# Optimization experiments

Hardware: AMD Instinct MI355X
Metric: run time of the kernel (lower is better)

## Reference

```python
import sys
import jax, jax.numpy as jnp
import numpy as np

sys.setrecursionlimit(100000)

MARGIN = 200.0
SAME_MARGIN = 0.0
REL_MARGIN = MARGIN - SAME_MARGIN  # margin - same_margin


def km_algorithm(mp):
    """Faithful numpy port of the repo's recursive Kuhn-Munkres (host-side,
    exactly mirroring the original CPU round-trip). mp: (n, n) float64.
    Returns transport plan T with T[link[y], y] = 1/n for matched pairs."""
    n = mp.shape[0]
    link = np.full(n, -1, dtype=np.int64)
    lx = mp.max(axis=1).astype(np.float64).copy()
    ly = np.zeros(n, dtype=np.float64)
    st = {}

    def dfs(x):
        st['visx'][x] = True
        for y in range(n):
            if st['visy'][y]:
                continue
            tmp = lx[x] + ly[y] - mp[x, y]
            if abs(tmp) < 1e-5:
                st['visy'][y] = True
                if link[y] == -1 or dfs(link[y]):
                    link[y] = x
                    return True
            elif st['sla'][y] + 1e-5 > tmp:
                st['sla'][y] = tmp
        return False

    for x in range(n):
        st['sla'] = np.full(n, 1e10, dtype=np.float64)
        while True:
            st['visx'] = np.zeros(n, dtype=bool)
            st['visy'] = np.zeros(n, dtype=bool)
            if dfs(x):
                break
            d = st['sla'][~st['visy']].min()
            lx[st['visx']] -= d
            ly[st['visy']] += d
            st['sla'][~st['visy']] -= d
    T = np.zeros((n, n), dtype=np.float64)
    for i in range(n):
        if link[i] != -1:
            T[link[i], i] = 1.0 / n
    return T


def sim_label(l1, l2):
    # (n, n) float: 1 where labels equal
    return (l1[:, None] == l2[None, :]).astype(jnp.float32)


def ground_metric(f1, f2, sim):
    # pairwise squared euclidean distances: ||a||^2 - 2 a.b + ||b||^2
    sq1 = jnp.sum(f1 * f1, axis=1)[:, None]
    sq2 = jnp.sum(f2 * f2, axis=1)[None, :]
    d2 = sq1 - 2.0 * (f1 @ f2.T) + sq2
    hinge_gm = jnp.maximum(0.0, SAME_MARGIN + REL_MARGIN - d2)   # negative pairs
    same_gm = jnp.maximum(0.0, d2 - SAME_MARGIN)                 # positive pairs
    return sim * same_gm + (1.0 - sim) * hinge_gm                # mode='both'


def setup_inputs() -> dict:
    key = jax.random.key(0)
    k1, k2, k3, k4 = jax.random.split(key, 4)
    n, d = 128, 8192
    return {
        "inputs_batch1": jax.random.normal(k1, (n, d), dtype=jnp.float32),
        "inputs_batch2": jax.random.normal(k2, (n, d), dtype=jnp.float32),
        "targets_batch1": jax.random.randint(k3, (n,), 0, 16, dtype=jnp.int64) if jax.config.jax_enable_x64 else jax.random.randint(k3, (n,), 0, 16).astype(jnp.int32),
        "targets_batch2": jax.random.randint(k4, (n,), 0, 16, dtype=jnp.int64) if jax.config.jax_enable_x64 else jax.random.randint(k4, (n,), 0, 16).astype(jnp.int32),
    }


def reference(inputs_batch1, inputs_batch2, targets_batch1, targets_batch2):
    sim = sim_label(targets_batch1, targets_batch2)
    GM = ground_metric(inputs_batch1, inputs_batch2, sim)
    # host round-trip for KM assignment, as in the original module
    T = km_algorithm(np.asarray(jax.device_get(GM), dtype=np.float64))
    T = jnp.asarray(T, dtype=jnp.float32)
    loss = jnp.sum(GM * T)
    return loss
```

## Files before the change

### kernel.cpp

```cpp
#include <hip/hip_runtime.h>

#define N 128
#define DIM 8192
#define NN (N * N)
#define ZSPLIT 64
#define NW 16
#define GSTRIDE 130

__device__ __forceinline__ void wave_fence() {
    __threadfence_block();
    __builtin_amdgcn_wave_barrier();
}
__device__ __forceinline__ double embed_key(double v, int j) {
    long long b = __double_as_longlong(v);
    return __longlong_as_double((b & ~127LL) | (long long)j);
}

__global__ __launch_bounds__(256) void d2_partial(const float* __restrict__ A,
                                                  const float* __restrict__ B,
                                                  float* __restrict__ d2p) {
    __shared__ float As[32][68];
    __shared__ float Bk[64][36];
    const int tid = threadIdx.x;
    const int bi = blockIdx.x, bj = blockIdx.y, bz = blockIdx.z;
    const int tx = tid & 15, ty = tid >> 4;
    const int row0 = bi * 32, col0 = bj * 32;
    const int kbase = bz * 128;
    float a00 = 0.f, a01 = 0.f, a10 = 0.f, a11 = 0.f;

    for (int it = 0; it < 2; ++it) {
        const int k0 = kbase + it * 64;
        __syncthreads();
        #pragma unroll
        for (int s = 0; s < 2; ++s) {
            int e = tid + s * 256;
            int r = e >> 4, q = e & 15;
            *(float4*)&As[r][q * 4] = *(const float4*)&A[(row0 + r) * DIM + k0 + q * 4];
        }
        #pragma unroll
        for (int s = 0; s < 2; ++s) {
            int r = tid & 31;
            int kq = (tid >> 5) + s * 8;
            float4 b4 = *(const float4*)&B[(col0 + r) * DIM + k0 + kq * 4];
            Bk[kq * 4 + 0][r] = b4.x;
            Bk[kq * 4 + 1][r] = b4.y;
            Bk[kq * 4 + 2][r] = b4.z;
            Bk[kq * 4 + 3][r] = b4.w;
        }
        __syncthreads();
        #pragma unroll
        for (int kk = 0; kk < 64; kk += 4) {
            float x0[4], x1[4];
            *(float4*)x0 = *(const float4*)&As[2 * ty][kk];
            *(float4*)x1 = *(const float4*)&As[2 * ty + 1][kk];
            float y[4][2];
            #pragma unroll
            for (int q = 0; q < 4; ++q)
                *(float2*)y[q] = *(const float2*)&Bk[kk + q][2 * tx];
            #pragma unroll
            for (int q = 0; q < 4; ++q) {
                float d;
                d = x0[q] - y[q][0]; a00 = fmaf(d, d, a00);
                d = x0[q] - y[q][1]; a01 = fmaf(d, d, a01);
                d = x1[q] - y[q][0]; a10 = fmaf(d, d, a10);
                d = x1[q] - y[q][1]; a11 = fmaf(d, d, a11);
            }
        }
    }
    const int o0 = (row0 + 2 * ty) * N + col0 + 2 * tx;
    float* dst = d2p + bz * NN;
    *(float2*)&dst[o0]     = make_float2(a00, a01);
    *(float2*)&dst[o0 + N] = make_float2(a10, a11);
}

__global__ __launch_bounds__(256) void reduce_gm(const float* __restrict__ d2p,
                                                 const int* __restrict__ t1,
                                                 const int* __restrict__ t2,
                                                 float* __restrict__ gm,
                                                 int* __restrict__ flagarr) {
    __shared__ int bf;
    if (threadIdx.x == 0) bf = 0;
    __syncthreads();
    const int o = blockIdx.x * 256 + threadIdx.x;
    float s0 = 0.f, s1 = 0.f, s2 = 0.f, s3 = 0.f, s4 = 0.f, s5 = 0.f, s6 = 0.f, s7 = 0.f;
    const float* p = d2p + o;
    #pragma unroll
    for (int z = 0; z < ZSPLIT; z += 8) {
        s0 += p[(z + 0) * NN]; s1 += p[(z + 1) * NN];
        s2 += p[(z + 2) * NN]; s3 += p[(z + 3) * NN];
        s4 += p[(z + 4) * NN]; s5 += p[(z + 5) * NN];
        s6 += p[(z + 6) * NN]; s7 += p[(z + 7) * NN];
    }
    float s = ((s0 + s1) + (s2 + s3)) + ((s4 + s5) + (s6 + s7));
    const int i = o >> 7, j = o & 127;
    const int l1 = t1[i], l2 = t2[j];
    const bool same = (l1 == l2);
    float g = same ? fmaxf(s, 0.f) : fmaxf(200.f - s, 0.f);
    gm[o] = g;
    bool bad = (!same && g > 0.f) || l1 < 0 || l1 > 63 || l2 < 0 || l2 > 63;
    unsigned long long m = __ballot(bad);
    if ((threadIdx.x & 63) == 0 && m) atomicOr(&bf, 1);
    __syncthreads();
    if (threadIdx.x == 0) flagarr[blockIdx.x] = bf;
}

__global__ __launch_bounds__(1024) void solve_kernel(const float* __restrict__ gm,
                                                     const int* __restrict__ flagarr,
                                                     const int* __restrict__ t1,
                                                     const int* __restrict__ t2,
                                                     float* __restrict__ out) {
    __shared__ float gml[N * GSTRIDE];
    __shared__ int lbl1[N], lbl2[N];
    __shared__ int rowlist[N], collist[N];
    __shared__ int rcnt[64], ccnt[64], rstart[65], cstart[65], rcur[64], ccur[64];
    __shared__ int tasks[65], bigtasks[65];
    __shared__ int ntasks_s, nbig_s, flag_s;
    __shared__ double totals[NW];
    __shared__ int claimw[NW][64];
    __shared__ double ub[N + 1], vbp[N + 1], minvb[N + 1];
    __shared__ int pb[N + 1], wayb[N + 1], usedb[N + 1];
    __shared__ double redv[NW];
    __shared__ int redi[NW];
    __shared__ double big_total;
    __shared__ int jfin_s;

    const int tid = threadIdx.x;
    if (tid < 64) { rcnt[tid] = 0; ccnt[tid] = 0; rcur[tid] = 0; ccur[tid] = 0; }
    if (tid == 0) { ntasks_s = 0; nbig_s = 0; flag_s = 0; big_total = 0.0; }
    if (tid < N)  { lbl1[tid] = t1[tid]; lbl2[tid] = t2[tid]; }
    __syncthreads();
    if (tid < 64 && flagarr[tid]) atomicOr(&flag_s, 1);
    if (tid < N) {
        atomicAdd(&rcnt[lbl1[tid] & 63], 1);
        atomicAdd(&ccnt[lbl2[tid] & 63], 1);
    }
    __syncthreads();
    if (tid < 64) {
        int rs_ = rcnt[tid], cs_ = ccnt[tid];
        #pragma unroll
        for (int o = 1; o < 64; o <<= 1) {
            int tr = __shfl_up(rs_, o, 64);
            int tc = __shfl_up(cs_, o, 64);
            if (tid >= o) { rs_ += tr; cs_ += tc; }
        }
        rstart[tid + 1] = rs_;
        cstart[tid + 1] = cs_;
        if (tid == 0) { rstart[0] = 0; cstart[0] = 0; }
        if (!flag_s) {
            int R = rcnt[tid], C = ccnt[tid];
            bool valid = (R > 0) && (C > 0);
            bool small = valid && (R <= 64) && (C <= 64);
            bool big   = valid && !small;
            unsigned long long ms = __ballot(small);
            unsigned long long mb = __ballot(big);
            if (small) tasks[__popcll(ms & ((1ull << tid) - 1))] = tid;
            if (big)   bigtasks[__popcll(mb & ((1ull << tid) - 1))] = tid;
            if (tid == 0) { ntasks_s = __popcll(ms); nbig_s = __popcll(mb); }
        } else if (tid == 0) { ntasks_s = 0; nbig_s = 1; bigtasks[0] = -1; }
    }
    __syncthreads();
    if (tid < N) {
        int l1 = lbl1[tid] & 63;
        int p = atomicAdd(&rcur[l1], 1);
        rowlist[rstart[l1] + p] = tid;
        int l2 = lbl2[tid] & 63;
        int q = atomicAdd(&ccur[l2], 1);
        collist[cstart[l2] + q] = tid;
    }
    __syncthreads();
    #pragma unroll
    for (int pch = 0; pch < 16; ++pch) {
        int e = tid + pch * 1024;
        int i = e >> 7, j = e & 127;
        gml[i * GSTRIDE + j] = gm[rowlist[i] * N + collist[j]];
    }
    __syncthreads();

    const int w = tid >> 6, lane = tid & 63;
    const int ntasks = ntasks_s;
    double acc = 0.0;

    for (int tk = w; tk < ntasks; tk += NW) {
        const int c = tasks[tk];
        const int Rn = rcnt[c], Cn = ccnt[c], rs = rstart[c], cs = cstart[c];
        const bool T  = (Rn > Cn);
        const int n_  = T ? Cn : Rn;
        const int m_  = T ? Rn : Cn;
        const int rstep = T ? 1 : GSTRIDE;
        const int cstep = T ? GSTRIDE : 1;
        const int rb00 = T ? cs : rs * GSTRIDE;
        const int ob00 = T ? rs * GSTRIDE : cs;
        int* clm = claimw[w];

        const bool cA = (lane < m_), rA = (lane < n_);
        const int myoff = ob00 + lane * cstep;
        const int myrb  = rb00 + lane * rstep;

        double u = 0.0;
        if (rA) {
            float mx = 0.f;
            int a = myrb + ob00;
            for (int j = 0; j < m_; ++j) { mx = fmaxf(mx, gml[a]); a += cstep; }
            u = -(double)mx;
        }
        double v = 1e30;
        {
            int a = rb00 + myoff;
            for (int i = 0; i < n_; ++i) {
                double ui = __shfl(u, i, 64);
                if (cA) v = fmin(v, -(double)gml[a] - ui);
                a += rstep;
            }
        }
        if (cA) clm[lane] = 0x7fffffff;
        wave_fence();
        int jc = -1;
        {
            int a = myrb + ob00;
            for (int j = 0; j < m_; ++j) {
                double vj = __shfl(v, j, 64);
                if (rA && jc < 0) {
                    double s = -(double)gml[a] - u - vj;
                    if (s < 1e-7) jc = j;
                }
                a += cstep;
            }
        }
        if (rA && jc >= 0) atomicMin(&clm[jc], lane);
        wave_fence();
        int p = -1;
        if (cA && clm[lane] != 0x7fffffff) p = clm[lane];
        bool rowm = (rA && jc >= 0 && clm[jc] == lane);

        for (int ir = 0; ir < n_; ++ir) {
            if (__shfl(rowm ? 1 : 0, ir, 64)) continue;
            double minv = 1e30, markD = -1.0, ent = -1.0;
            bool used = false; int way = -2;
            if (rA && lane == ir) ent = 0.0;
            double D = 0.0;
            int i0 = ir, jprev = -1;
            int guard = 2 * m_ + 8;
            while (guard-- > 0) {
                double ui = __shfl(u, i0, 64);
                int rb = rb00 + i0 * rstep;
                if (cA && !used) {
                    double cand = D - ui - (double)gml[rb + myoff] - v;
                    if (cand < minv) { minv = cand; way = jprev; }
                }
                double kd = (cA && !used) ? embed_key(minv, lane) : 1e30;
                #pragma unroll
                for (int o = 1; o < 64; o <<= 1) kd = fmin(kd, __shfl_xor(kd, o, 64));
                long long kb = __double_as_longlong(kd);
                int j1 = (int)(kb & 127);
                double Dn = __longlong_as_double(kb & ~127LL);
                if (Dn > 1e29) break;
                D = Dn;
                int i1 = __shfl(p, j1, 64);
                if (i1 < 0) {
                    int jj = j1;
                    while (true) {
                        int wp = __shfl(way, jj, 64);
                        int pn = (wp < 0) ? ir : __shfl(p, wp, 64);
                        if (cA && lane == jj) p = pn;
                        if (wp < 0) break;
                        jj = wp;
                    }
                    if (rA && lane == ir) rowm = true;
                    break;
                }
                if (cA && lane == j1) { used = true; markD = D; }
                if (rA && lane == i1) ent = D;
                jprev = j1; i0 = i1;
            }
            if (rA && ent   >= 0.0) u += D - ent;
            if (cA && markD >= 0.0) v -= D - markD;
        }

        double val = 0.0;
        if (cA && p >= 0) val = (double)gml[rb00 + p * rstep + myoff];
        #pragma unroll
        for (int o = 1; o < 64; o <<= 1) val += __shfl_xor(val, o, 64);
        acc += val;
    }
    if (lane == 0) totals[w] = acc;
    __syncthreads();

    const int nbig = nbig_s;
    for (int bt = 0; bt < nbig; ++bt) {
        const int c = bigtasks[bt];
        int Rn, Cn, rs, cs;
        if (c < 0) { Rn = N; Cn = N; rs = 0; cs = 0; }
        else { Rn = rcnt[c]; Cn = ccnt[c]; rs = rstart[c]; cs = cstart[c]; }
        const bool T = (Rn > Cn);
        const int n_ = T ? Cn : Rn, m_ = T ? Rn : Cn;
        const int rstep = T ? 1 : GSTRIDE;
        const int cstep = T ? GSTRIDE : 1;
        const int rb00 = T ? cs : rs * GSTRIDE;
        const int ob00 = T ? rs * GSTRIDE : cs;
        auto cost = [&](int i, int j) -> double {
            return -(double)gml[rb00 + i * rstep + ob00 + j * cstep];
        };
        for (int x = tid; x <= m_; x += 1024) { vbp[x] = 0.0; pb[x] = 0; }
        for (int x = tid; x <= n_; x += 1024) { ub[x] = 0.0; }
        __syncthreads();
        for (int i = 1; i <= n_; ++i) {
            if (tid == 0) pb[0] = i;
            for (int x = tid; x <= m_; x += 1024) { minvb[x] = 1e300; usedb[x] = 0; }
            __syncthreads();
            int j0 = 0;
            int guard = 2 * m_ + 8;
            while (guard-- > 0) {
                if (tid == 0) usedb[j0] = 1;
                __syncthreads();
                const int i0 = pb[j0];
                double dl = 1e300; int jl = 0;
                if (tid < m_) {
                    int j = tid + 1;
                    if (!usedb[j]) {
                        double cur = cost(i0 - 1, j - 1) - ub[i0] - vbp[j];
                        if (cur < minvb[j]) { minvb[j] = cur; wayb[j] = j0; }
                        dl = minvb[j]; jl = j;
                    }
                }
                double rv = dl; int ri = jl;
                #pragma unroll
                for (int o = 32; o > 0; o >>= 1) {
                    double ov = __shfl_down(rv, o, 64);
                    int oi2 = __shfl_down(ri, o, 64);
                    if (ov < rv) { rv = ov; ri = oi2; }
                }
                if ((tid & 63) == 0) { redv[tid >> 6] = rv; redi[tid >> 6] = ri; }
                __syncthreads();
                if (tid == 0) {
                    double bd = 1e300; int bj = 0;
                    for (int q = 0; q < NW; ++q) if (redv[q] < bd) { bd = redv[q]; bj = redi[q]; }
                    redv[0] = bd; redi[0] = bj;
                }
                __syncthreads();
                const double delta = redv[0];
                const int j1 = redi[0];
                if (tid < m_) {
                    int j = tid + 1;
                    if (usedb[j]) { ub[pb[j]] += delta; vbp[j] -= delta; }
                    else          { minvb[j] -= delta; }
                }
                if (tid == 0) ub[pb[0]] += delta;
                __syncthreads();
                j0 = j1;
                if (pb[j0] == 0) break;
            }
            if (tid == 0) jfin_s = j0;
            __syncthreads();
            if (tid == 0) {
                int jj = jfin_s;
                while (jj) { int jp = wayb[jj]; pb[jj] = pb[jp]; jj = jp; }
            }
            __syncthreads();
        }
        double bl = 0.0;
        if (tid < m_) { int j = tid + 1; if (pb[j] != 0) bl = -cost(pb[j] - 1, j - 1); }
        #pragma unroll
        for (int o = 32; o > 0; o >>= 1) bl += __shfl_down(bl, o, 64);
        if ((tid & 63) == 0) redv[tid >> 6] = bl;
        __syncthreads();
        if (tid == 0) { double s = 0; for (int q = 0; q < NW; ++q) s += redv[q]; big_total += s; }
        __syncthreads();
    }

    if (tid == 0) {
        double s = big_total;
        for (int i = 0; i < NW; ++i) s += totals[i];
        out[0] = (float)(s / (double)N);
    }
}

extern "C" void kernel_launch(void* const* d_in, const int* in_sizes, int n_in,
                              void* d_out, int out_size, void* d_ws, size_t ws_size,
                              hipStream_t stream) {
    const float* A  = (const float*)d_in[0];
    const float* B  = (const float*)d_in[1];
    const int*   t1 = (const int*)d_in[2];
    const int*   t2 = (const int*)d_in[3];
    float* out = (float*)d_out;
    float* d2p = (float*)d_ws;
    float* gm  = (float*)d_ws + ZSPLIT * NN;
    int*   flagarr = (int*)(gm + NN);

    d2_partial<<<dim3(4, 4, ZSPLIT), 256, 0, stream>>>(A, B, d2p);
    reduce_gm<<<64, 256, 0, stream>>>(d2p, t1, t2, gm, flagarr);
    solve_kernel<<<1, 1024, 0, stream>>>(gm, flagarr, t1, t2, out);
}
```

Measured before the change: 90.61 us.

## Use 64x64 tiles with 4x4 register microtiles and finer K split

The squared-distance partial kernel now gives each block a 64x64 output tile over a 64-wide K slice. It loads that slice once and accumulates a 4x4 register microtile per thread, instead of 32x32 tiles with 2x2 microtiles over two 64-wide K steps. The K split grows from 64 to 128 slices and the grid becomes a flat 512 blocks. This halves global reads of A and B and raises arithmetic intensity per shared-memory load. In exchange, the partial-sum buffer doubles, so the reduction kernel reads twice as many partials through new tile-aware indexing.

```diff
diff --git a/kernel.cpp b/kernel.cpp
--- a/kernel.cpp
+++ b/kernel.cpp
@@ -3,7 +3,7 @@
 #define N 128
 #define DIM 8192
 #define NN (N * N)
-#define ZSPLIT 64
+#define ZS 128
 #define NW 16
 #define GSTRIDE 130
 
@@ -19,58 +19,58 @@
 __global__ __launch_bounds__(256) void d2_partial(const float* __restrict__ A,
                                                   const float* __restrict__ B,
                                                   float* __restrict__ d2p) {
-    __shared__ float As[32][68];
-    __shared__ float Bk[64][36];
+    __shared__ float As[64][68];
+    __shared__ float Bk[64][68];
     const int tid = threadIdx.x;
-    const int bi = blockIdx.x, bj = blockIdx.y, bz = blockIdx.z;
+    const int b = blockIdx.x;
+    const int bi = b & 1, bj = (b >> 1) & 1, bz = b >> 2;
+    const int row0 = bi * 64, col0 = bj * 64, k0 = bz * 64;
+
+    #pragma unroll
+    for (int s = 0; s < 4; ++s) {
+        int e = tid + s * 256;
+        int r = e >> 4, q = e & 15;
+        *(float4*)&As[r][q * 4] = *(const float4*)&A[(row0 + r) * DIM + k0 + q * 4];
+    }
+    #pragma unroll
+    for (int s = 0; s < 4; ++s) {
+        int e = tid + s * 256;
+        int c = e & 63, kq = e >> 6;
+        float4 b4 = *(const float4*)&B[(col0 + c) * DIM + k0 + kq * 4];
+        Bk[kq * 4 + 0][c] = b4.x;
+        Bk[kq * 4 + 1][c] = b4.y;
+        Bk[kq * 4 + 2][c] = b4.z;
+        Bk[kq * 4 + 3][c] = b4.w;
+    }
+    __syncthreads();
+
     const int tx = tid & 15, ty = tid >> 4;
-    const int row0 = bi * 32, col0 = bj * 32;
-    const int kbase = bz * 128;
-    float a00 = 0.f, a01 = 0.f, a10 = 0.f, a11 = 0.f;
-
-    for (int it = 0; it < 2; ++it) {
-        const int k0 = kbase + it * 64;
-        __syncthreads();
-        #pragma unroll
-        for (int s = 0; s < 2; ++s) {
-            int e = tid + s * 256;
-            int r = e >> 4, q = e & 15;
-            *(float4*)&As[r][q * 4] = *(const float4*)&A[(row0 + r) * DIM + k0 + q * 4];
-        }
-        #pragma unroll
-        for (int s = 0; s < 2; ++s) {
-            int r = tid & 31;
-            int kq = (tid >> 5) + s * 8;
-            float4 b4 = *(const float4*)&B[(col0 + r) * DIM + k0 + kq * 4];
-            Bk[kq * 4 + 0][r] = b4.x;
-            Bk[kq * 4 + 1][r] = b4.y;
-            Bk[kq * 4 + 2][r] = b4.z;
-            Bk[kq * 4 + 3][r] = b4.w;
-        }
-        __syncthreads();
-        #pragma unroll
-        for (int kk = 0; kk < 64; kk += 4) {
-            float x0[4], x1[4];
-            *(float4*)x0 = *(const float4*)&As[2 * ty][kk];
-            *(float4*)x1 = *(const float4*)&As[2 * ty + 1][kk];
-            float y[4][2];
-            #pragma unroll
-            for (int q = 0; q < 4; ++q)
-                *(float2*)y[q] = *(const float2*)&Bk[kk + q][2 * tx];
+    float acc[4][4] = {};
+    #pragma unroll
+    for (int kk = 0; kk < 64; kk += 4) {
+        float a[4][4], bb[4][4];
+        #pragma unroll
+        for (int i = 0; i < 4; ++i)
+            *(float4*)a[i] = *(const float4*)&As[4 * ty + i][kk];
+        #pragma unroll
+        for (int q = 0; q < 4; ++q)
+            *(float4*)bb[q] = *(const float4*)&Bk[kk + q][4 * tx];
+        #pragma unroll
+        for (int i = 0; i < 4; ++i)
             #pragma unroll
             for (int q = 0; q < 4; ++q) {
-                float d;
-                d = x0[q] - y[q][0]; a00 = fmaf(d, d, a00);
-                d = x0[q] - y[q][1]; a01 = fmaf(d, d, a01);
-                d = x1[q] - y[q][0]; a10 = fmaf(d, d, a10);
-                d = x1[q] - y[q][1]; a11 = fmaf(d, d, a11);
-            }
-        }
-    }
-    const int o0 = (row0 + 2 * ty) * N + col0 + 2 * tx;
-    float* dst = d2p + bz * NN;
-    *(float2*)&dst[o0]     = make_float2(a00, a01);
-    *(float2*)&dst[o0 + N] = make_float2(a10, a11);
+                float av = a[i][q];
+                #pragma unroll
+                for (int j = 0; j < 4; ++j) {
+                    float d = av - bb[q][j];
+                    acc[i][j] = fmaf(d, d, acc[i][j]);
+                }
+            }
+    }
+    float* dst = d2p + b * 4096;
+    #pragma unroll
+    for (int i = 0; i < 4; ++i)
+        *(float4*)&dst[(4 * ty + i) * 64 + 4 * tx] = *(float4*)acc[i];
 }
 
 __global__ __launch_bounds__(256) void reduce_gm(const float* __restrict__ d2p,
@@ -82,17 +82,19 @@
     if (threadIdx.x == 0) bf = 0;
     __syncthreads();
     const int o = blockIdx.x * 256 + threadIdx.x;
+    const int i = o >> 7, j = o & 127;
+    const int tilebase = (((j >> 6) << 1) | (i >> 6)) * 4096;
+    const int inner = (i & 63) * 64 + (j & 63);
+    const float* p = d2p + tilebase + inner;
     float s0 = 0.f, s1 = 0.f, s2 = 0.f, s3 = 0.f, s4 = 0.f, s5 = 0.f, s6 = 0.f, s7 = 0.f;
-    const float* p = d2p + o;
-    #pragma unroll
-    for (int z = 0; z < ZSPLIT; z += 8) {
-        s0 += p[(z + 0) * NN]; s1 += p[(z + 1) * NN];
-        s2 += p[(z + 2) * NN]; s3 += p[(z + 3) * NN];
-        s4 += p[(z + 4) * NN]; s5 += p[(z + 5) * NN];
-        s6 += p[(z + 6) * NN]; s7 += p[(z + 7) * NN];
+    #pragma unroll
+    for (int z = 0; z < ZS; z += 8) {
+        s0 += p[(z + 0) * 16384]; s1 += p[(z + 1) * 16384];
+        s2 += p[(z + 2) * 16384]; s3 += p[(z + 3) * 16384];
+        s4 += p[(z + 4) * 16384]; s5 += p[(z + 5) * 16384];
+        s6 += p[(z + 6) * 16384]; s7 += p[(z + 7) * 16384];
     }
     float s = ((s0 + s1) + (s2 + s3)) + ((s4 + s5) + (s6 + s7));
-    const int i = o >> 7, j = o & 127;
     const int l1 = t1[i], l2 = t2[j];
     const bool same = (l1 == l2);
     float g = same ? fmaxf(s, 0.f) : fmaxf(200.f - s, 0.f);
@@ -383,10 +385,10 @@
     const int*   t2 = (const int*)d_in[3];
     float* out = (float*)d_out;
     float* d2p = (float*)d_ws;
-    float* gm  = (float*)d_ws + ZSPLIT * NN;
+    float* gm  = (float*)d_ws + ZS * 4 * 4096;
     int*   flagarr = (int*)(gm + NN);
 
-    d2_partial<<<dim3(4, 4, ZSPLIT), 256, 0, stream>>>(A, B, d2p);
+    d2_partial<<<ZS * 4, 256, 0, stream>>>(A, B, d2p);
     reduce_gm<<<64, 256, 0, stream>>>(d2p, t1, t2, gm, flagarr);
     solve_kernel<<<1, 1024, 0, stream>>>(gm, flagarr, t1, t2, out);
 }
```

Result: no change. 92.40 us (+2.0%).
